# Kernel optimization log

Measured on AMD Instinct MI355X. Metric: run time of the kernel, lower is better.

The kernel has to match this reference:

```python
import jax, jax.numpy as jnp
import numpy as np

N = 8192
SQUARE_SIZE = 10.0
NEIGHBOURHOOD = 1.0
THRESHOLD = 1.0
DECAY = 0.9


def setup_inputs() -> dict:
    key = jax.random.key(0)
    k1, k2, k3, k4 = jax.random.split(key, 4)
    # Random 2D topology on a square, as in SpikingLayer.__init__
    topo = jax.random.uniform(k1, (N, 2), dtype=jnp.float32) * SQUARE_SIZE
    # Pairwise squared distances without the [N,N,2] intermediate
    sq = jnp.sum(topo * topo, axis=1)  # [N]
    d2 = sq[:, None] + sq[None, :] - 2.0 * (topo @ topo.T)  # [N,N]
    mask = (d2 <= NEIGHBOURHOOD * NEIGHBOURHOOD).astype(jnp.float32)
    # Per-node weight rows, zeroed outside the neighbourhood radius
    W = jax.random.normal(k2, (N, N), dtype=jnp.float32) * mask
    # Random initial firing state (0/1) so dynamics are non-trivial
    f0 = (jax.random.uniform(k3, (N,)) > 0.5).astype(jnp.float32)
    v0 = jnp.zeros((N,), dtype=jnp.float32)
    x = jax.random.normal(k4, (N,), dtype=jnp.float32)  # unused, as in torch forward
    return {"W": W, "f0": f0, "v0": v0, "x": x, "num_steps": 64}


def reference(W, f0, v0, x, num_steps):
    # One scan step == one call to SpikingLayer.forward():
    #   node_x = W @ is_firing  (fused over all nodes)
    #   LIF update: v = decay*v + node_x; spike if v >= threshold; reset on spike
    def step(carry, _):
        v, f = carry
        u = W @ f                      # [N] weighted input from firing neighbours
        v = DECAY * v + u
        spike = v >= THRESHOLD         # bool [N]
        f_new = spike.astype(v.dtype)
        v = jnp.where(spike, 0.0, v)   # reset fired neurons
        return (v, f_new), f_new

    (_, _), firing_matrix = jax.lax.scan(step, (v0, f0), None, length=num_steps)
    return firing_matrix  # [num_steps, N], the accumulated firing_matrix
```

## Files before the change

kernel.cpp:

```cpp
#include <hip/hip_runtime.h>

#define NN 8192
#define STEPS 64
#define DECAYF 0.9f
#define THRESHF 1.0f
#define K_MAX 384
#define K_SEG 192
#define KITER 24

#define CBLOCKS 256
#define STHREADS 576
#define MBSTRIDE 16

typedef unsigned long long u64;
typedef unsigned int u32;

__device__ __forceinline__ void pub_store(u64* p, u64 v) {
    __hip_atomic_store(p, v, __ATOMIC_RELAXED, __HIP_MEMORY_SCOPE_AGENT);
}
__device__ __forceinline__ u64 pub_load(const u64* p) {
    return __hip_atomic_load(p, __ATOMIC_RELAXED, __HIP_MEMORY_SCOPE_AGENT);
}

__global__ __launch_bounds__(256) void extract_ell(
        const float* __restrict__ W,
        u64* __restrict__ pk) {
    const int wave = threadIdx.x >> 6;
    const int lane = threadIdx.x & 63;
    const int hrow = blockIdx.x * 4 + wave;
    const int row  = hrow >> 1;
    const int half = hrow & 1;
    const int cbase = half * (NN / 2);

    const float4* wr4 = (const float4*)(W + (size_t)row * NN + cbase);
    u64* pr = pk + (size_t)row * K_MAX + half * K_SEG;
    const u64 lmask = (1ull << lane) - 1ull;

    int base = 0;
    for (int c4 = lane; c4 < NN / 8; c4 += 64) {
        float4 w = wr4[c4];
        const int col0 = cbase + c4 * 4;
        #pragma unroll
        for (int comp = 0; comp < 4; ++comp) {
            float val = (comp == 0) ? w.x : (comp == 1) ? w.y
                      : (comp == 2) ? w.z : w.w;
            u64 m = __ballot(val != 0.0f);
            if (val != 0.0f) {
                int idx = base + __popcll(m & lmask);
                if (idx < K_SEG)
                    pr[idx] = ((u64)(u32)(col0 + comp) << 32)
                            | (u64)__float_as_uint(val);
            }
            base += __popcll(m);
        }
    }
    const int cap = (base < K_SEG) ? base : K_SEG;
    for (int j = cap + lane; j < K_SEG; j += 64) pr[j] = 0ull;
}

__global__ __launch_bounds__(STHREADS) void spiking_steps(
        const u64* __restrict__ pk,
        const float* __restrict__ f0,
        const float* __restrict__ v0,
        float* __restrict__ out,
        u64* __restrict__ fdata) {
    __shared__ u32 lds_fbits[2][CBLOCKS];
    __shared__ u32 lds_spike[8];
    __shared__ int lds_cnt[STEPS];
    __shared__ int lds_flag;

    const int tid  = threadIdx.x;
    const int wave = tid >> 6;
    const int lane = tid & 63;
    const int bid  = blockIdx.x;

    if (tid < STEPS) lds_cnt[tid] = 0;
    if (tid == 0) lds_flag = 0;

    if (wave == 0) {
        float f = (lane < 32) ? f0[bid * 32 + lane] : 0.0f;
        u64 m = __ballot(f != 0.0f);
        if (lane == 0)
            pub_store(&fdata[(size_t)bid * MBSTRIDE],
                      (1ull << 32) | (u32)(m & 0xffffffffull));
    }
    __syncthreads();

    if (wave == 0) {
        for (int s = 0; s < STEPS; ++s) {
            const u64* slot = fdata + (size_t)(s & 1) * CBLOCKS * MBSTRIDE;
            const u32 want = (u32)(s + 1);
            u32* fb = lds_fbits[s & 1];
            u32 pend = 0xFu;
            for (;;) {
                #pragma unroll
                for (int k = 0; k < 4; ++k) {
                    if ((pend >> k) & 1u) {
                        u64 w = pub_load(&slot[(size_t)(lane + 64 * k) * MBSTRIDE]);
                        if ((u32)(w >> 32) == want) {
                            fb[lane + 64 * k] = (u32)w;
                            pend &= ~(1u << k);
                        }
                    }
                }
                if (__all(pend == 0)) break;
                __builtin_amdgcn_s_sleep(2);
            }
            if (lane == 0)
                __hip_atomic_store(&lds_flag, s + 1, __ATOMIC_RELEASE,
                                   __HIP_MEMORY_SCOPE_WORKGROUP);
        }
    } else {
        const int g    = wave - 1;
        const int rloc = g * 4 + (lane >> 4);
        const int row  = bid * 32 + rloc;
        const int l16  = lane & 15;

        u32 ecol[KITER]; float eval[KITER];
        const u64* pr = pk + (size_t)row * K_MAX;
        #pragma unroll
        for (int k = 0; k < KITER; ++k) {
            u64 p = pr[l16 + 16 * k];
            ecol[k] = (u32)(p >> 32);
            eval[k] = __uint_as_float((u32)p);
        }
        float vreg = v0[row];

        for (int s = 0; s < STEPS; ++s) {
            while (__hip_atomic_load(&lds_flag, __ATOMIC_ACQUIRE,
                                     __HIP_MEMORY_SCOPE_WORKGROUP) < s + 1) {}
            const u32* fb = lds_fbits[s & 1];

            double a0 = 0.0, a1 = 0.0, a2 = 0.0;
            #pragma unroll
            for (int k = 0; k < KITER; k += 3) {
                u32 c0 = ecol[k],     w0 = fb[c0 >> 5];
                u32 c1 = ecol[k + 1], w1 = fb[c1 >> 5];
                u32 c2 = ecol[k + 2], w2 = fb[c2 >> 5];
                a0 += (double)(((w0 >> (c0 & 31)) & 1u) ? eval[k]     : 0.0f);
                a1 += (double)(((w1 >> (c1 & 31)) & 1u) ? eval[k + 1] : 0.0f);
                a2 += (double)(((w2 >> (c2 & 31)) & 1u) ? eval[k + 2] : 0.0f);
            }
            double acc = (a0 + a1) + a2;
            #pragma unroll
            for (int m = 8; m >= 1; m >>= 1)
                acc += __shfl_xor(acc, m, 64);

            float u  = (float)acc;
            float vv = __fadd_rn(__fmul_rn(DECAYF, vreg), u);
            int fire = (vv >= THRESHF);
            vreg = fire ? 0.0f : vv;

            u64 bal = __ballot(fire);
            int old = -1;
            if (lane == 0) {
                u32 bits4 = ((u32)(bal       ) & 1u)
                          | (((u32)(bal >> 16) & 1u) << 1)
                          | (((u32)(bal >> 32) & 1u) << 2)
                          | (((u32)(bal >> 48) & 1u) << 3);
                __hip_atomic_store(&lds_spike[g], bits4, __ATOMIC_RELAXED,
                                   __HIP_MEMORY_SCOPE_WORKGROUP);
                old = __hip_atomic_fetch_add(&lds_cnt[s], 1, __ATOMIC_ACQ_REL,
                                             __HIP_MEMORY_SCOPE_WORKGROUP);
            }
            old = __shfl(old, 0, 64);
            if (old == 7) {
                u32 b = (lane < 8) ? ((lds_spike[lane] & 0xFu) << (4 * lane)) : 0u;
                b |= __shfl_xor(b, 1, 64);
                b |= __shfl_xor(b, 2, 64);
                b |= __shfl_xor(b, 4, 64);
                if (lane == 0)
                    pub_store(&fdata[((size_t)((s + 1) & 1) * CBLOCKS + bid) * MBSTRIDE],
                              ((u64)(u32)(s + 2) << 32) | b);
            }

            if (l16 == 0)
                out[(size_t)s * NN + row] = fire ? 1.0f : 0.0f;
        }
    }
}

extern "C" void kernel_launch(void* const* d_in, const int* in_sizes, int n_in,
                              void* d_out, int out_size, void* d_ws, size_t ws_size,
                              hipStream_t stream) {
    const float* W  = (const float*)d_in[0];
    const float* f0 = (const float*)d_in[1];
    const float* v0 = (const float*)d_in[2];
    float* out = (float*)d_out;

    u64* pk    = (u64*)d_ws;
    u64* fdata = pk + (size_t)NN * K_MAX;

    extract_ell<<<dim3(NN * 2 / 4), dim3(256), 0, stream>>>(W, pk);
    spiking_steps<<<dim3(CBLOCKS), dim3(STHREADS), 0, stream>>>(
        pk, f0, v0, out, fdata);
}
```

Before: 556.9 us.

## Fuse ELL extraction into spiking kernel via LDS staging

Result: no change. 558.7 us (+0.3%).

```diff
diff --git a/kernel.cpp b/kernel.cpp
--- a/kernel.cpp
+++ b/kernel.cpp
@@ -7,6 +7,8 @@
 #define K_MAX 384
 #define K_SEG 192
 #define KITER 24
+#define LROWS 32
+#define LPITCH 385
 
 #define CBLOCKS 256
 #define STHREADS 576
@@ -22,48 +24,13 @@
     return __hip_atomic_load(p, __ATOMIC_RELAXED, __HIP_MEMORY_SCOPE_AGENT);
 }
 
-__global__ __launch_bounds__(256) void extract_ell(
+__global__ __launch_bounds__(STHREADS) void spiking_fused(
         const float* __restrict__ W,
-        u64* __restrict__ pk) {
-    const int wave = threadIdx.x >> 6;
-    const int lane = threadIdx.x & 63;
-    const int hrow = blockIdx.x * 4 + wave;
-    const int row  = hrow >> 1;
-    const int half = hrow & 1;
-    const int cbase = half * (NN / 2);
-
-    const float4* wr4 = (const float4*)(W + (size_t)row * NN + cbase);
-    u64* pr = pk + (size_t)row * K_MAX + half * K_SEG;
-    const u64 lmask = (1ull << lane) - 1ull;
-
-    int base = 0;
-    for (int c4 = lane; c4 < NN / 8; c4 += 64) {
-        float4 w = wr4[c4];
-        const int col0 = cbase + c4 * 4;
-        #pragma unroll
-        for (int comp = 0; comp < 4; ++comp) {
-            float val = (comp == 0) ? w.x : (comp == 1) ? w.y
-                      : (comp == 2) ? w.z : w.w;
-            u64 m = __ballot(val != 0.0f);
-            if (val != 0.0f) {
-                int idx = base + __popcll(m & lmask);
-                if (idx < K_SEG)
-                    pr[idx] = ((u64)(u32)(col0 + comp) << 32)
-                            | (u64)__float_as_uint(val);
-            }
-            base += __popcll(m);
-        }
-    }
-    const int cap = (base < K_SEG) ? base : K_SEG;
-    for (int j = cap + lane; j < K_SEG; j += 64) pr[j] = 0ull;
-}
-
-__global__ __launch_bounds__(STHREADS) void spiking_steps(
-        const u64* __restrict__ pk,
         const float* __restrict__ f0,
         const float* __restrict__ v0,
         float* __restrict__ out,
         u64* __restrict__ fdata) {
+    __shared__ u64 lds_ell[LROWS * LPITCH];
     __shared__ u32 lds_fbits[2][CBLOCKS];
     __shared__ u32 lds_spike[8];
     __shared__ int lds_cnt[STEPS];
@@ -83,6 +50,44 @@
         if (lane == 0)
             pub_store(&fdata[(size_t)bid * MBSTRIDE],
                       (1ull << 32) | (u32)(m & 0xffffffffull));
+    }
+
+    {
+        const u64 lmask = (1ull << lane) - 1ull;
+        for (int hr = wave; hr < 2 * LROWS; hr += 9) {
+            const int rloc = hr >> 1;
+            const int half = hr & 1;
+            const int cbase = half * (NN / 2);
+            const float4* wr4 = (const float4*)
+                (W + (size_t)(bid * LROWS + rloc) * NN + cbase);
+            u64* pr = lds_ell + rloc * LPITCH + half * K_SEG;
+
+            float4 wv[16];
+            #pragma unroll
+            for (int i = 0; i < 16; ++i)
+                wv[i] = wr4[lane + 64 * i];
+
+            int base = 0;
+            #pragma unroll
+            for (int i = 0; i < 16; ++i) {
+                const int col0 = cbase + (lane + 64 * i) * 4;
+                #pragma unroll
+                for (int comp = 0; comp < 4; ++comp) {
+                    float val = (comp == 0) ? wv[i].x : (comp == 1) ? wv[i].y
+                              : (comp == 2) ? wv[i].z : wv[i].w;
+                    u64 m = __ballot(val != 0.0f);
+                    if (val != 0.0f) {
+                        int idx = base + __popcll(m & lmask);
+                        if (idx < K_SEG)
+                            pr[idx] = ((u64)(u32)(col0 + comp) << 32)
+                                    | (u64)__float_as_uint(val);
+                    }
+                    base += __popcll(m);
+                }
+            }
+            const int cap = (base < K_SEG) ? base : K_SEG;
+            for (int j = cap + lane; j < K_SEG; j += 64) pr[j] = 0ull;
+        }
     }
     __syncthreads();
 
@@ -113,11 +118,11 @@
     } else {
         const int g    = wave - 1;
         const int rloc = g * 4 + (lane >> 4);
-        const int row  = bid * 32 + rloc;
+        const int row  = bid * LROWS + rloc;
         const int l16  = lane & 15;
 
         u32 ecol[KITER]; float eval[KITER];
-        const u64* pr = pk + (size_t)row * K_MAX;
+        const u64* pr = lds_ell + rloc * LPITCH;
         #pragma unroll
         for (int k = 0; k < KITER; ++k) {
             u64 p = pr[l16 + 16 * k];
@@ -188,10 +193,8 @@
     const float* v0 = (const float*)d_in[2];
     float* out = (float*)d_out;
 
-    u64* pk    = (u64*)d_ws;
-    u64* fdata = pk + (size_t)NN * K_MAX;
-
-    extract_ell<<<dim3(NN * 2 / 4), dim3(256), 0, stream>>>(W, pk);
-    spiking_steps<<<dim3(CBLOCKS), dim3(STHREADS), 0, stream>>>(
-        pk, f0, v0, out, fdata);
-}
+    u64* fdata = (u64*)d_ws;
+
+    spiking_fused<<<dim3(CBLOCKS), dim3(STHREADS), 0, stream>>>(
+        W, f0, v0, out, fdata);
+}
```
